# Optimization experiments

Measured on AMD Instinct MI355X. Metric: run time of the kernel, lower is better.

Reference implementation:

```python
import jax, jax.numpy as jnp
import numpy as np

NUM_KEYS = 8192
NUM_BINS = 128
NUM_FREQS = 64
NUM_KERNELS = 3
HEAD_DIM = 2 * NUM_FREQS


def setup_inputs() -> dict:
    key = jax.random.key(0)
    k1, k2, k3, k4, k5 = jax.random.split(key, 5)
    fan_in = NUM_FREQS * NUM_KERNELS
    bound = np.sqrt(6.0 / fan_in)
    return {
        "K": jax.random.normal(k1, (NUM_KEYS, HEAD_DIM), dtype=jnp.float32),
        "reference_angles": jax.random.normal(k2, (NUM_FREQS,), dtype=jnp.float32),
        "mu": jax.random.uniform(k3, (NUM_BINS, NUM_FREQS, NUM_KERNELS), minval=-1.0, maxval=1.0, dtype=jnp.float32),
        "kappa": jax.random.uniform(k4, (NUM_BINS, NUM_FREQS, NUM_KERNELS), minval=0.0, maxval=1.0, dtype=jnp.float32),
        "weight": jax.random.uniform(k5, (NUM_BINS, NUM_FREQS, NUM_KERNELS), minval=-bound, maxval=bound, dtype=jnp.float32),
        "bias": jnp.zeros((NUM_BINS,), dtype=jnp.float32),
    }


def reference(K, reference_angles, mu, kappa, weight, bias):
    n = K.shape[0]
    num_bins, num_freqs, num_kernels = mu.shape
    # split head_dim into (freq, 2) complex pairs
    Kc = K.reshape(n, num_freqs, 2)                      # (n, f, 2)
    magnitude = jnp.sqrt(jnp.sum(Kc * Kc, axis=2))       # (n, f)
    angle = jnp.arctan2(Kc[..., 1], Kc[..., 0])          # (n, f)
    # shift kernel centers by per-round reference angles
    mu_eff = mu + reference_angles[None, :, None]        # (b, f, k)
    # von Mises kernel: exp(kappa * (cos(angle - mu) - 1))
    # broadcast to (n, b, f, k) -- this is the fat intermediate
    delta = angle[:, None, :, None] - mu_eff[None]       # (n, b, f, k)
    kernel = jnp.exp(kappa[None] * (jnp.cos(delta) - 1.0))
    # sum over kernels with weights, then over freqs with magnitude
    wk = jnp.einsum('nbfk,bfk->nbf', kernel, weight)     # (n, b, f)
    logits = jnp.einsum('nbf,nf->nb', wk, magnitude)     # (n, b)
    return logits + bias[None, :]
```

## Files before the change

kernel.cpp:

```cpp
#include <hip/hip_runtime.h>
#include <math.h>

#define NKEYS 8192
#define NBINS 128
#define NFREQ 64
#define NKER  3
#define HEADD 128

#define MHARM 6
#define NCH   (2 * MHARM + 1)
#define KDIM  (NCH * NFREQ)
#define KSTEPS (KDIM / 32)

typedef _Float16 f16x8 __attribute__((ext_vector_type(8)));
typedef float    f32x4 __attribute__((ext_vector_type(4)));

#define FRAG_KT(ch, f) ((ch) * 2 + ((f) >> 5))
#define FRAG_Q(f)      (((f) >> 3) & 3)
#define FRAG_J(f)      ((f) & 7)

__global__ void build_coeffs(const float* __restrict__ refang,
                             const float* __restrict__ mu,
                             const float* __restrict__ kappa,
                             const float* __restrict__ weight,
                             _Float16* __restrict__ Bswz) {
    int gid = blockIdx.x * blockDim.x + threadIdx.x;
    if (gid >= NBINS * NFREQ) return;
    int b = gid >> 6, f = gid & 63;
    float rf = refang[f];

    float acc[NCH];
    #pragma unroll
    for (int c = 0; c < NCH; ++c) acc[c] = 0.f;

    #pragma unroll
    for (int k = 0; k < NKER; ++k) {
        int idx = (b * NFREQ + f) * NKER + k;
        float me  = mu[idx] + rf;
        float kap = kappa[idx];
        float w   = weight[idx];
        float h = 0.5f * kap, h2 = h * h;
        float wek = w * __expf(-kap);
        float c1, s1;
        __sincosf(me, &s1, &c1);

        float Im[MHARM + 1];
        float tm = 1.f;
        #pragma unroll
        for (int m = 0; m <= MHARM; ++m) {
            float t = tm, s = tm;
            #pragma unroll
            for (int j = 1; j <= 6; ++j) { t *= h2 / (float)(j * (m + j)); s += t; }
            Im[m] = s;
            tm *= h / (float)(m + 1);
        }

        acc[0] += wek * Im[0];
        float cp = 1.f, sp = 0.f, cc = c1, sc = s1;
        #pragma unroll
        for (int m = 1; m <= MHARM; ++m) {
            float g = 2.f * wek * Im[m];
            acc[2 * m - 1] += g * cc;
            acc[2 * m]     += g * sc;
            float cn = fmaf(2.f * c1, cc, -cp);
            float sn = fmaf(2.f * c1, sc, -sp);
            cp = cc; sp = sc; cc = cn; sc = sn;
        }
    }

    const int colgrp = b >> 4, lc = b & 15;
    const int q = FRAG_Q(f), j = FRAG_J(f);
    #pragma unroll
    for (int c = 0; c < NCH; ++c) {
        int kt = FRAG_KT(c, f);
        Bswz[((size_t)(colgrp * KSTEPS + kt) * 64 + q * 16 + lc) * 8 + j] = (_Float16)acc[c];
    }
}

#define BM 16
#define GTHREADS 512

__global__ __launch_bounds__(GTHREADS) void fused_gemm(
    const float* __restrict__ K,
    const _Float16* __restrict__ Bswz,
    const float* __restrict__ bias,
    float* __restrict__ out)
{
    __shared__ __align__(16) _Float16 Afrag[KSTEPS * 64 * 8];

    const int tid  = threadIdx.x;
    const int row0 = blockIdx.x * BM;

    for (int p = tid; p < BM * NFREQ; p += GTHREADS) {
        int n = p >> 6, f = p & 63;
        const float2 xy = *(const float2*)(K + (size_t)(row0 + n) * HEADD + 2 * f);
        float m2   = xy.x * xy.x + xy.y * xy.y;
        float rinv = (m2 > 0.f) ? rsqrtf(m2) : 0.f;
        float mag  = m2 * rinv;
        float c1   = xy.x * rinv, s1 = xy.y * rinv;
        const int q = FRAG_Q(f), j = FRAG_J(f);
        Afrag[FRAG_KT(0, f) * 512 + (q * 16 + n) * 8 + j] = (_Float16)mag;
        float cp = 1.f, sp = 0.f, cc = c1, sc = s1;
        #pragma unroll
        for (int m = 1; m <= MHARM; ++m) {
            Afrag[FRAG_KT(2 * m - 1, f) * 512 + (q * 16 + n) * 8 + j] = (_Float16)(mag * cc);
            Afrag[FRAG_KT(2 * m, f)     * 512 + (q * 16 + n) * 8 + j] = (_Float16)(mag * sc);
            float cn = fmaf(2.f * c1, cc, -cp);
            float sn = fmaf(2.f * c1, sc, -sp);
            cp = cc; sp = sc; cc = cn; sc = sn;
        }
    }
    __syncthreads();

    const int lane = tid & 63, wave = tid >> 6;
    const int lc = lane & 15, q = lane >> 4;
    const int col = wave * 16 + lc;

    f32x4 acc = {0.f, 0.f, 0.f, 0.f};

    const f16x8* bp = (const f16x8*)Bswz + (size_t)wave * KSTEPS * 64 + lane;
    const f16x8* ap = (const f16x8*)Afrag + lane;

    #pragma unroll
    for (int kt = 0; kt < KSTEPS; ++kt) {
        f16x8 b = bp[kt * 64];
        f16x8 a = ap[kt * 64];
        acc = __builtin_amdgcn_mfma_f32_16x16x32_f16(a, b, acc, 0, 0, 0);
    }

    const float bb = bias[col];
    #pragma unroll
    for (int j = 0; j < 4; ++j)
        out[(size_t)(row0 + q * 4 + j) * NBINS + col] = acc[j] + bb;
}

#define KPB 16
#define FTHREADS 512
#define KPT 4
#define KV_STRIDE (KPB + 1)
#define LOG2E 1.44269504088896340736f

__global__ __launch_bounds__(FTHREADS) void vonmises_fallback(
    const float* __restrict__ K,
    const float* __restrict__ refang,
    const float* __restrict__ mu,
    const float* __restrict__ kappa,
    const float* __restrict__ weight,
    const float* __restrict__ bias,
    float* __restrict__ out)
{
    __shared__ float4 kvlds[NFREQ * KV_STRIDE];
    const int tid  = threadIdx.x;
    const int key0 = blockIdx.x * KPB;

    for (int p = tid; p < KPB * NFREQ; p += FTHREADS) {
        int key = p >> 6, f = p & (NFREQ - 1);
        const float2 xy = *(const float2*)(K + (size_t)(key0 + key) * HEADD + 2 * f);
        float m2 = xy.x * xy.x + xy.y * xy.y;
        float rm = (m2 > 0.f) ? rsqrtf(m2) : 0.f;
        kvlds[f * KV_STRIDE + key] = make_float4(xy.x * rm, xy.y * rm, m2 * rm, 0.f);
    }
    __syncthreads();

    const int bin = tid & (NBINS - 1);
    const int kbase = (tid >> 7) * KPT;
    float acc[KPT] = {0.f, 0.f, 0.f, 0.f};

    for (int f = 0; f < NFREQ; ++f) {
        float4 kv[KPT];
        #pragma unroll
        for (int j = 0; j < KPT; ++j) kv[j] = kvlds[f * KV_STRIDE + kbase + j];
        float wk[KPT] = {0.f, 0.f, 0.f, 0.f};
        #pragma unroll
        for (int k = 0; k < NKER; ++k) {
            int idx = (bin * NFREQ + f) * NKER + k;
            float me = mu[idx] + refang[f];
            float ka = kappa[idx] * LOG2E;
            float s, c;
            __sincosf(me, &s, &c);
            #pragma unroll
            for (int j = 0; j < KPT; ++j) {
                float t = fmaf(kv[j].x, ka * c, fmaf(kv[j].y, ka * s, -ka));
                wk[j] = fmaf(exp2f(t), weight[idx], wk[j]);
            }
        }
        #pragma unroll
        for (int j = 0; j < KPT; ++j) acc[j] = fmaf(wk[j], kv[j].z, acc[j]);
    }
    const float bb = bias[bin];
    #pragma unroll
    for (int j = 0; j < KPT; ++j)
        out[(size_t)(key0 + kbase + j) * NBINS + bin] = acc[j] + bb;
}

extern "C" void kernel_launch(void* const* d_in, const int* in_sizes, int n_in,
                              void* d_out, int out_size, void* d_ws, size_t ws_size,
                              hipStream_t stream) {
    const float* K      = (const float*)d_in[0];
    const float* refang = (const float*)d_in[1];
    const float* mu     = (const float*)d_in[2];
    const float* kappa  = (const float*)d_in[3];
    const float* weight = (const float*)d_in[4];
    const float* bias   = (const float*)d_in[5];
    float* out = (float*)d_out;

    const size_t need = (size_t)NBINS * KDIM * sizeof(_Float16);

    if (ws_size >= need) {
        _Float16* Bswz = (_Float16*)d_ws;
        build_coeffs<<<NBINS * NFREQ / 64, 64, 0, stream>>>(
            refang, mu, kappa, weight, Bswz);
        fused_gemm<<<NKEYS / BM, GTHREADS, 0, stream>>>(K, Bswz, bias, out);
    } else {
        vonmises_fallback<<<NKEYS / KPB, FTHREADS, 0, stream>>>(
            K, refang, mu, kappa, weight, bias, out);
    }
}
```

Baseline: 17.14 us.

## Cut Fourier harmonics to four and retile fused GEMM with two row chunks per block

This lowers the harmonic truncation from 6 to 4, which shrinks the GEMM K dimension from 832 to 576. It also restructures fused_gemm: each block now handles 32 rows and half of the bin columns, every wave runs two MFMAs that share one B fragment, B loads are software-prefetched, and the A-fragment build uses vectorized float4 loads and f16x4 LDS stores. build_coeffs switches to 256-thread blocks. Dropping harmonics reduces accuracy of the von Mises expansion for larger kappa, and each K-row feature block is now computed twice, once per column-half block.

```diff
diff --git a/kernel.cpp b/kernel.cpp
--- a/kernel.cpp
+++ b/kernel.cpp
@@ -7,12 +7,13 @@
 #define NKER  3
 #define HEADD 128
 
-#define MHARM 6
+#define MHARM 4
 #define NCH   (2 * MHARM + 1)
 #define KDIM  (NCH * NFREQ)
 #define KSTEPS (KDIM / 32)
 
 typedef _Float16 f16x8 __attribute__((ext_vector_type(8)));
+typedef _Float16 f16x4 __attribute__((ext_vector_type(4)));
 typedef float    f32x4 __attribute__((ext_vector_type(4)));
 
 #define FRAG_KT(ch, f) ((ch) * 2 + ((f) >> 5))
@@ -68,70 +69,106 @@
         }
     }
 
-    const int colgrp = b >> 4, lc = b & 15;
+    const int g = b >> 4, lc = b & 15;
     const int q = FRAG_Q(f), j = FRAG_J(f);
     #pragma unroll
     for (int c = 0; c < NCH; ++c) {
         int kt = FRAG_KT(c, f);
-        Bswz[((size_t)(colgrp * KSTEPS + kt) * 64 + q * 16 + lc) * 8 + j] = (_Float16)acc[c];
-    }
-}
-
-#define BM 16
-#define GTHREADS 512
-
-__global__ __launch_bounds__(GTHREADS) void fused_gemm(
+        Bswz[((size_t)(g * KSTEPS + kt) * 64 + q * 16 + lc) * 8 + j] = (_Float16)acc[c];
+    }
+}
+
+#define BM 32
+#define GT 256
+
+__global__ __launch_bounds__(GT, 4) void fused_gemm(
     const float* __restrict__ K,
     const _Float16* __restrict__ Bswz,
     const float* __restrict__ bias,
     float* __restrict__ out)
 {
-    __shared__ __align__(16) _Float16 Afrag[KSTEPS * 64 * 8];
+    __shared__ __align__(16) _Float16 Afrag[2 * KSTEPS * 512];
 
     const int tid  = threadIdx.x;
-    const int row0 = blockIdx.x * BM;
-
-    for (int p = tid; p < BM * NFREQ; p += GTHREADS) {
-        int n = p >> 6, f = p & 63;
-        const float2 xy = *(const float2*)(K + (size_t)(row0 + n) * HEADD + 2 * f);
-        float m2   = xy.x * xy.x + xy.y * xy.y;
-        float rinv = (m2 > 0.f) ? rsqrtf(m2) : 0.f;
-        float mag  = m2 * rinv;
-        float c1   = xy.x * rinv, s1 = xy.y * rinv;
-        const int q = FRAG_Q(f), j = FRAG_J(f);
-        Afrag[FRAG_KT(0, f) * 512 + (q * 16 + n) * 8 + j] = (_Float16)mag;
-        float cp = 1.f, sp = 0.f, cc = c1, sc = s1;
+    const int bid  = blockIdx.x;
+    const int row0 = (bid >> 1) * BM;
+    const int cblk = bid & 1;
+
+    #pragma unroll
+    for (int it = 0; it < 2; ++it) {
+        const int qi = tid + it * GT;
+        const int n  = qi >> 4;
+        const int f0 = (qi & 15) * 4;
+        const float* kp = K + (size_t)(row0 + n) * HEADD + 2 * f0;
+        const float4 p0 = *(const float4*)kp;
+        const float4 p1 = *(const float4*)(kp + 4);
+        float xs[4] = {p0.x, p0.z, p1.x, p1.z};
+        float ys[4] = {p0.y, p0.w, p1.y, p1.w};
+        float mag[4], c1[4], s1[4], cc[4], sc[4], cp[4], sp[4];
+        #pragma unroll
+        for (int i = 0; i < 4; ++i) {
+            float m2 = xs[i] * xs[i] + ys[i] * ys[i];
+            float ri = (m2 > 0.f) ? rsqrtf(m2) : 0.f;
+            mag[i] = m2 * ri; c1[i] = xs[i] * ri; s1[i] = ys[i] * ri;
+            cp[i] = 1.f; sp[i] = 0.f; cc[i] = c1[i]; sc[i] = s1[i];
+        }
+        const int chunk = n >> 4, lc = n & 15;
+        const int q = FRAG_Q(f0), j0 = FRAG_J(f0);
+        _Float16* base = Afrag + chunk * (KSTEPS * 512) + (q * 16 + lc) * 8 + j0;
+        f16x4 v;
+        #pragma unroll
+        for (int i = 0; i < 4; ++i) v[i] = (_Float16)mag[i];
+        *(f16x4*)(base + FRAG_KT(0, f0) * 512) = v;
         #pragma unroll
         for (int m = 1; m <= MHARM; ++m) {
-            Afrag[FRAG_KT(2 * m - 1, f) * 512 + (q * 16 + n) * 8 + j] = (_Float16)(mag * cc);
-            Afrag[FRAG_KT(2 * m, f)     * 512 + (q * 16 + n) * 8 + j] = (_Float16)(mag * sc);
-            float cn = fmaf(2.f * c1, cc, -cp);
-            float sn = fmaf(2.f * c1, sc, -sp);
-            cp = cc; sp = sc; cc = cn; sc = sn;
+            f16x4 vc, vs;
+            #pragma unroll
+            for (int i = 0; i < 4; ++i) {
+                vc[i] = (_Float16)(mag[i] * cc[i]);
+                vs[i] = (_Float16)(mag[i] * sc[i]);
+            }
+            *(f16x4*)(base + FRAG_KT(2 * m - 1, f0) * 512) = vc;
+            *(f16x4*)(base + FRAG_KT(2 * m, f0)     * 512) = vs;
+            #pragma unroll
+            for (int i = 0; i < 4; ++i) {
+                float cn = fmaf(2.f * c1[i], cc[i], -cp[i]);
+                float sn = fmaf(2.f * c1[i], sc[i], -sp[i]);
+                cp[i] = cc[i]; sp[i] = sc[i]; cc[i] = cn; sc[i] = sn;
+            }
         }
     }
     __syncthreads();
 
     const int lane = tid & 63, wave = tid >> 6;
     const int lc = lane & 15, q = lane >> 4;
-    const int col = wave * 16 + lc;
-
-    f32x4 acc = {0.f, 0.f, 0.f, 0.f};
-
-    const f16x8* bp = (const f16x8*)Bswz + (size_t)wave * KSTEPS * 64 + lane;
-    const f16x8* ap = (const f16x8*)Afrag + lane;
-
+    const int g = cblk * 4 + wave;
+    const int col = g * 16 + lc;
+
+    f32x4 acc0 = {0.f, 0.f, 0.f, 0.f};
+    f32x4 acc1 = {0.f, 0.f, 0.f, 0.f};
+
+    const f16x8* bp  = (const f16x8*)Bswz + (size_t)g * KSTEPS * 64 + lane;
+    const f16x8* ap0 = (const f16x8*)Afrag + lane;
+    const f16x8* ap1 = ap0 + KSTEPS * 64;
+
+    f16x8 b = bp[0];
     #pragma unroll
     for (int kt = 0; kt < KSTEPS; ++kt) {
-        f16x8 b = bp[kt * 64];
-        f16x8 a = ap[kt * 64];
-        acc = __builtin_amdgcn_mfma_f32_16x16x32_f16(a, b, acc, 0, 0, 0);
+        f16x8 bn = b;
+        if (kt + 1 < KSTEPS) bn = bp[(kt + 1) * 64];
+        f16x8 a0 = ap0[kt * 64];
+        f16x8 a1 = ap1[kt * 64];
+        acc0 = __builtin_amdgcn_mfma_f32_16x16x32_f16(a0, b, acc0, 0, 0, 0);
+        acc1 = __builtin_amdgcn_mfma_f32_16x16x32_f16(a1, b, acc1, 0, 0, 0);
+        b = bn;
     }
 
     const float bb = bias[col];
     #pragma unroll
-    for (int j = 0; j < 4; ++j)
-        out[(size_t)(row0 + q * 4 + j) * NBINS + col] = acc[j] + bb;
+    for (int j = 0; j < 4; ++j) {
+        out[(size_t)(row0 + q * 4 + j) * NBINS + col]      = acc0[j] + bb;
+        out[(size_t)(row0 + 16 + q * 4 + j) * NBINS + col] = acc1[j] + bb;
+    }
 }
 
 #define KPB 16
@@ -208,9 +245,9 @@
 
     if (ws_size >= need) {
         _Float16* Bswz = (_Float16*)d_ws;
-        build_coeffs<<<NBINS * NFREQ / 64, 64, 0, stream>>>(
+        build_coeffs<<<NBINS * NFREQ / 256, 256, 0, stream>>>(
             refang, mu, kappa, weight, Bswz);
-        fused_gemm<<<NKEYS / BM, GTHREADS, 0, stream>>>(K, Bswz, bias, out);
+        fused_gemm<<<(NKEYS / BM) * 2, GT, 0, stream>>>(K, Bswz, bias, out);
     } else {
         vonmises_fallback<<<NKEYS / KPB, FTHREADS, 0, stream>>>(
             K, refang, mu, kappa, weight, bias, out);
```

New measurement: 16.18 us. -5.6%, faster.
